# Kernel optimization log

Hardware: AMD Instinct MI355X
Metric: run time of the kernel (lower is better)

## Reference

```python
import jax, jax.numpy as jnp
import numpy as np

NUM_HEADS = 16
INACTIVE = 4          # cfg_comp.attention_heads_inactive
SIG_DIM = 64          # cfg_comp.attention_heads_signature_dim
MLP_HIDDEN = 512      # cfg_comp.attention_heads_inference_mlp_hidden


def setup_inputs() -> dict:
    key = jax.random.key(0)
    ks = jax.random.split(key, 16)
    S, B, E = 2048, 2, 1024
    def xavier(k, shape, gain=1.0):
        fan_in, fan_out = shape[1], shape[0]
        a = gain * np.sqrt(6.0 / (fan_in + fan_out))
        return jax.random.uniform(k, shape, jnp.float32, -a, a)
    g = 1.0 / np.sqrt(2.0)
    return {
        "query": jax.random.normal(ks[0], (S, B, E), jnp.float32),
        "q_w": xavier(ks[1], (E, E), g), "q_b": jnp.zeros((E,), jnp.float32),
        "k_w": xavier(ks[2], (E, E), g), "k_b": jnp.zeros((E,), jnp.float32),
        "v_w": xavier(ks[3], (E, E), g), "v_b": jnp.zeros((E,), jnp.float32),
        "out_w": xavier(ks[4], (E, E)), "out_b": jnp.zeros((E,), jnp.float32),
        "inf1_w": xavier(ks[5], (MLP_HIDDEN, E), np.sqrt(2.0)),
        "inf1_b": jnp.zeros((MLP_HIDDEN,), jnp.float32),
        "inf2_w": xavier(ks[6], (SIG_DIM, MLP_HIDDEN), np.sqrt(2.0)),
        "inf2_b": jnp.zeros((SIG_DIM,), jnp.float32),
        "head_sig": jax.random.normal(ks[7], (NUM_HEADS, SIG_DIM), jnp.float32)
                    * np.sqrt(2.0 / (NUM_HEADS + SIG_DIM)),
    }


def _head_mask(query, inf1_w, inf1_b, inf2_w, inf2_b, head_sig):
    # inference_masking_step: (S, B, E) -> binary mask (B, H, S)
    t = jax.nn.relu(query @ inf1_w.T + inf1_b)          # (S, B, hidden)
    t = t @ inf2_w.T + inf2_b                            # (S, B, sig)
    s = t @ head_sig.T                                   # (S, B, H) head scores
    keep = NUM_HEADS - INACTIVE
    kth = jax.lax.top_k(s, keep)[0][..., -1]             # (S, B) kth-largest score
    mask = (s >= kth[..., None]).astype(query.dtype)     # 1 at top-`keep` heads
    mask = jax.lax.stop_gradient(mask)                   # scatter of constants in torch
    return jnp.transpose(mask, (1, 2, 0))                # (B, H, S)


def reference(query, q_w, q_b, k_w, k_b, v_w, v_b, out_w, out_b,
              inf1_w, inf1_b, inf2_w, inf2_b, head_sig):
    S, B, E = query.shape
    H, D = NUM_HEADS, E // NUM_HEADS
    scaling = D ** (-0.5)

    q = (query @ q_w.T + q_b) * scaling                  # (S, B, E)
    k = query @ k_w.T + k_b
    v = query @ v_w.T + v_b
    # (S, B, E) -> (B, H, S, D)
    to_bhsd = lambda x: jnp.transpose(x.reshape(S, B, H, D), (1, 2, 0, 3))
    q, k, v = to_bhsd(q), to_bhsd(k), to_bhsd(v)

    attn = jax.nn.softmax(jnp.einsum("bhqd,bhkd->bhqk", q, k), axis=-1)
    o = jnp.einsum("bhqk,bhkd->bhqd", attn, v)           # (B, H, S, D)

    mask = _head_mask(query, inf1_w, inf1_b, inf2_w, inf2_b, head_sig)  # (B, H, S)
    o = o * mask[..., None]                              # gate per head per position

    out = jnp.transpose(o, (2, 0, 1, 3)).reshape(S, B, E)
    return out @ out_w.T + out_b
```

## Files before the change

kernel.cpp:

```cpp
#include <hip/hip_runtime.h>
#include <hip/hip_bf16.h>

#define S_LEN 2048
#define BATCH 2
#define EDIM 1024
#define NHEAD 16
#define DHEAD 64
#define HIDDEN 512
#define SIGD 64
#define KEEP 12

typedef __attribute__((ext_vector_type(8))) short bf16x8;
typedef __attribute__((ext_vector_type(4))) float f32x4;

static __device__ __forceinline__ float bf2f(short s) {
  unsigned int u = ((unsigned int)(unsigned short)s) << 16;
  float f; __builtin_memcpy(&f, &u, 4); return f;
}
static __device__ __forceinline__ short f2bf(float f) {
  unsigned int u; __builtin_memcpy(&u, &f, 4);
  u += 0x7fffu + ((u >> 16) & 1u);
  return (short)(u >> 16);
}

#if __has_builtin(__builtin_amdgcn_exp2f)
static __device__ __forceinline__ float fexp2(float x) { return __builtin_amdgcn_exp2f(x); }
#else
static __device__ __forceinline__ float fexp2(float x) { return exp2f(x); }
#endif

static __device__ __forceinline__ void gl_lds16(const short* g, short* l) {
  __builtin_amdgcn_global_load_lds(
      (const __attribute__((address_space(1))) unsigned int*)g,
      (__attribute__((address_space(3))) unsigned int*)l, 16, 0, 0);
}

template<int CTRL>
static __device__ __forceinline__ float dpp_movf(float x) {
  return __builtin_bit_cast(float, __builtin_amdgcn_update_dpp(
      0, __builtin_bit_cast(int, x), CTRL, 0xF, 0xF, true));
}
static __device__ __forceinline__ float row_max16(float v) {
  v = fmaxf(v, dpp_movf<0x128>(v));
  v = fmaxf(v, dpp_movf<0x124>(v));
  v = fmaxf(v, dpp_movf<0x122>(v));
  v = fmaxf(v, dpp_movf<0x121>(v));
  return v;
}
static __device__ __forceinline__ float row_sum16(float v) {
  v += dpp_movf<0x128>(v);
  v += dpp_movf<0x124>(v);
  v += dpp_movf<0x122>(v);
  v += dpp_movf<0x121>(v);
  return v;
}

__global__ __launch_bounds__(256) void cvt_all(
    const float* __restrict__ query, const float* __restrict__ inf1_w,
    const float* __restrict__ qw, const float* __restrict__ kw,
    const float* __restrict__ vw, const float* __restrict__ ow,
    short* __restrict__ qh, short* __restrict__ ql,
    short* __restrict__ w1h, short* __restrict__ w1l,
    short* __restrict__ Wq, short* __restrict__ Wk,
    short* __restrict__ Wv, short* __restrict__ Wo)
{
  int blk = blockIdx.x;
  if (blk < 4608) {
    const float* in; short *oh, *ol; int i;
    if (blk < 4096) { in = query;  oh = qh;  ol = ql;  i = (blk * 256 + threadIdx.x) * 4; }
    else            { in = inf1_w; oh = w1h; ol = w1l; i = ((blk - 4096) * 256 + threadIdx.x) * 4; }
    float4 f = *(const float4*)(in + i);
    union { short s[4]; uint2 v; } uh, ul;
    float x[4] = {f.x, f.y, f.z, f.w};
    #pragma unroll
    for (int u = 0; u < 4; ++u) {
      short h = f2bf(x[u]);
      uh.s[u] = h;
      ul.s[u] = f2bf(x[u] - bf2f(h));
    }
    *(uint2*)(oh + i) = uh.v;
    *(uint2*)(ol + i) = ul.v;
  } else {
    int t = blk - 4608;
    int mat = t >> 10, sub = t & 1023;
    const float* in = (mat == 0) ? qw : (mat == 1) ? kw : (mat == 2) ? vw : ow;
    short* out      = (mat == 0) ? Wq : (mat == 1) ? Wk : (mat == 2) ? Wv : Wo;
    int i = (sub * 256 + threadIdx.x) * 4;
    float4 f = *(const float4*)(in + i);
    union { short s[4]; uint2 v; } u;
    u.s[0] = f2bf(f.x); u.s[1] = f2bf(f.y); u.s[2] = f2bf(f.z); u.s[3] = f2bf(f.w);
    *(uint2*)(out + i) = u.v;
  }
}

template<bool F32OUT>
static __device__ __forceinline__ void gemm128_body(
    short* smem,
    const short* __restrict__ A, const short* __restrict__ B,
    const float* __restrict__ bias, void* __restrict__ outv,
    int row0, int col0, float scale)
{
  short* As = smem;
  short* Bs = smem + 128*32;
  const int tid  = threadIdx.x;
  const int wave = tid >> 6, lane = tid & 63;
  const int quad = lane >> 4, l16 = lane & 15;
  const int wr = wave >> 1, wc = wave & 1;
  const int lr = lane >> 2, lc8 = (lane & 3) * 8;

  const short* gA = A + (size_t)(row0 + wave*16 + lr) * EDIM + lc8;
  const short* gB = B + (size_t)(col0 + wave*16 + lr) * EDIM + lc8;
  short* lA = As + wave*512;
  short* lB = Bs + wave*512;

  f32x4 acc[4][4] = {};
  gl_lds16(gA, lA);  gl_lds16(gA + 64*EDIM, lA + 64*32);
  gl_lds16(gB, lB);  gl_lds16(gB + 64*EDIM, lB + 64*32);

  for (int k0 = 0; k0 < EDIM; k0 += 32) {
    __syncthreads();
    bf16x8 af[4], bfr[4];
    #pragma unroll
    for (int i = 0; i < 4; ++i)
      af[i] = *(const bf16x8*)&As[(wr*64 + i*16 + l16)*32 + quad*8];
    #pragma unroll
    for (int j = 0; j < 4; ++j)
      bfr[j] = *(const bf16x8*)&Bs[(wc*64 + j*16 + l16)*32 + quad*8];
    __syncthreads();
    if (k0 + 32 < EDIM) {
      const short* gA2 = gA + k0 + 32;
      const short* gB2 = gB + k0 + 32;
      gl_lds16(gA2, lA);  gl_lds16(gA2 + 64*EDIM, lA + 64*32);
      gl_lds16(gB2, lB);  gl_lds16(gB2 + 64*EDIM, lB + 64*32);
    }
    #pragma unroll
    for (int i = 0; i < 4; ++i)
      #pragma unroll
      for (int j = 0; j < 4; ++j)
        acc[i][j] = __builtin_amdgcn_mfma_f32_16x16x32_bf16(af[i], bfr[j], acc[i][j], 0, 0, 0);
  }
  #pragma unroll
  for (int j = 0; j < 4; ++j) {
    int col = col0 + wc*64 + j*16 + l16;
    float bv = bias[col];
    #pragma unroll
    for (int i = 0; i < 4; ++i) {
      int rowb = row0 + wr*64 + i*16 + quad*4;
      #pragma unroll
      for (int r = 0; r < 4; ++r) {
        float v = (acc[i][j][r] + bv) * scale;
        if constexpr (F32OUT) {
          ((float*)outv)[(size_t)(rowb + r) * EDIM + col] = v;
        } else {
          ((short*)outv)[(size_t)(rowb + r) * EDIM + col] = f2bf(v);
        }
      }
    }
  }
}

static __device__ __forceinline__ void gemm_t1_body(
    short* smem,
    const short* __restrict__ Agh, const short* __restrict__ Agl,
    const short* __restrict__ Bgh, const short* __restrict__ Bgl,
    const float* __restrict__ bias, float* __restrict__ T1,
    int row0, int col0)
{
  short* Ah = smem;
  short* Al = smem + 4096;
  short* Bh = smem + 8192;
  short* Bl = smem + 10240;
  const int tid  = threadIdx.x;
  const int wave = tid >> 6, lane = tid & 63;
  const int quad = lane >> 4, l16 = lane & 15;
  const int wr = wave >> 1, wc = wave & 1;
  const int lr = lane >> 2, lc8 = (lane & 3) * 8;

  const short* gAh = Agh + (size_t)(row0 + wave*16 + lr) * EDIM + lc8;
  const short* gAl = Agl + (size_t)(row0 + wave*16 + lr) * EDIM + lc8;
  const short* gBh = Bgh + (size_t)(col0 + wave*16 + lr) * EDIM + lc8;
  const short* gBl = Bgl + (size_t)(col0 + wave*16 + lr) * EDIM + lc8;
  short* lAh = Ah + wave*512;  short* lAl = Al + wave*512;
  short* lBh = Bh + wave*512;  short* lBl = Bl + wave*512;

  f32x4 acc[4][2] = {};
  gl_lds16(gAh, lAh);  gl_lds16(gAh + 64*EDIM, lAh + 64*32);
  gl_lds16(gAl, lAl);  gl_lds16(gAl + 64*EDIM, lAl + 64*32);
  gl_lds16(gBh, lBh);  gl_lds16(gBl, lBl);

  for (int k0 = 0; k0 < EDIM; k0 += 32) {
    __syncthreads();
    bf16x8 ah[4], al[4], bh[2], bl[2];
    #pragma unroll
    for (int i = 0; i < 4; ++i) {
      ah[i] = *(const bf16x8*)&Ah[(wr*64 + i*16 + l16)*32 + quad*8];
      al[i] = *(const bf16x8*)&Al[(wr*64 + i*16 + l16)*32 + quad*8];
    }
    #pragma unroll
    for (int j = 0; j < 2; ++j) {
      bh[j] = *(const bf16x8*)&Bh[(wc*32 + j*16 + l16)*32 + quad*8];
      bl[j] = *(const bf16x8*)&Bl[(wc*32 + j*16 + l16)*32 + quad*8];
    }
    __syncthreads();
    if (k0 + 32 < EDIM) {
      const short* p;
      p = gAh + k0 + 32;  gl_lds16(p, lAh);  gl_lds16(p + 64*EDIM, lAh + 64*32);
      p = gAl + k0 + 32;  gl_lds16(p, lAl);  gl_lds16(p + 64*EDIM, lAl + 64*32);
      gl_lds16(gBh + k0 + 32, lBh);  gl_lds16(gBl + k0 + 32, lBl);
    }
    #pragma unroll
    for (int i = 0; i < 4; ++i)
      #pragma unroll
      for (int j = 0; j < 2; ++j) {
        acc[i][j] = __builtin_amdgcn_mfma_f32_16x16x32_bf16(ah[i], bh[j], acc[i][j], 0, 0, 0);
        acc[i][j] = __builtin_amdgcn_mfma_f32_16x16x32_bf16(ah[i], bl[j], acc[i][j], 0, 0, 0);
        acc[i][j] = __builtin_amdgcn_mfma_f32_16x16x32_bf16(al[i], bh[j], acc[i][j], 0, 0, 0);
      }
  }
  #pragma unroll
  for (int j = 0; j < 2; ++j) {
    int col = col0 + wc*32 + j*16 + l16;
    float bv = bias[col];
    #pragma unroll
    for (int i = 0; i < 4; ++i) {
      int rowb = row0 + wr*64 + i*16 + quad*4;
      #pragma unroll
      for (int r = 0; r < 4; ++r)
        T1[(size_t)(rowb + r) * HIDDEN + col] = fmaxf(acc[i][j][r] + bv, 0.0f);
    }
  }
}

__global__ __launch_bounds__(256) void mega_gemm1(
    const short* __restrict__ qh, const short* __restrict__ ql,
    const short* __restrict__ w1h, const short* __restrict__ w1l,
    const float* __restrict__ inf1_b, float* __restrict__ T1,
    const short* __restrict__ Wq, const short* __restrict__ Wk,
    const short* __restrict__ Wv,
    const float* __restrict__ qb, const float* __restrict__ kb,
    const float* __restrict__ vb,
    short* __restrict__ Qp, short* __restrict__ Kp, short* __restrict__ Vp)
{
  __shared__ __attribute__((aligned(16))) short smem[12288];
  int blk = blockIdx.x;
  if ((blk & 3) == 3) {
    int id = blk >> 2;
    gemm_t1_body(smem, qh, ql, w1h, w1l, inf1_b, T1,
                 (id & 31) * 128, (id >> 5) * 64);
  } else {
    int id = (blk >> 2) * 3 + (blk & 3);
    int row0 = (id & 31) * 128;
    int rest = id >> 5;
    int mat = rest >> 3, cb = rest & 7;
    const short* B   = (mat == 0) ? Wq : (mat == 1) ? Wk : Wv;
    const float* bia = (mat == 0) ? qb : (mat == 1) ? kb : vb;
    short* out       = (mat == 0) ? Qp : (mat == 1) ? Kp : Vp;
    float scale      = (mat == 0) ? 0.18033688011112042f : 1.0f;
    gemm128_body<false>(smem, qh, B, bia, (void*)out, row0, cb * 128, scale);
  }
}

__global__ __launch_bounds__(256) void mid_kernel(
    const float* __restrict__ T1, const float* __restrict__ inf2_w,
    const float* __restrict__ inf2_b, const float* __restrict__ head_sig,
    float* __restrict__ maskbuf,
    const short* __restrict__ Vp, short* __restrict__ VT)
{
  __shared__ __attribute__((aligned(16))) float fsm[16*HIDDEN + 16*SIGD + 16*NHEAD];
  int blk = blockIdx.x;
  const int tid = threadIdx.x;
  if (blk < 256) {
    float (*t1s)[HIDDEN] = (float(*)[HIDDEN])fsm;
    float (*t2s)[SIGD]   = (float(*)[SIGD])(fsm + 16*HIDDEN);
    float (*ss)[NHEAD]   = (float(*)[NHEAD])(fsm + 16*HIDDEN + 16*SIGD);
    const int tok0 = blk * 16;
    {
      int row = tid >> 4, c0 = (tid & 15) * 32;
      const float* src = T1 + (size_t)(tok0 + row) * HIDDEN + c0;
      #pragma unroll
      for (int u = 0; u < 8; ++u)
        *(float4*)&t1s[row][c0 + u*4] = *(const float4*)(src + u*4);
    }
    __syncthreads();
    #pragma unroll
    for (int it = 0; it < 4; ++it) {
      int idx = tid + it * 256;
      int tok = idx >> 6, j = idx & 63;
      const float4* w4 = (const float4*)(inf2_w + (size_t)j * HIDDEN);
      const float4* t4 = (const float4*)(&t1s[tok][0]);
      float a = inf2_b[j];
      for (int k = 0; k < HIDDEN/4; ++k) {
        float4 wv = w4[k], tv = t4[k];
        a += tv.x*wv.x + tv.y*wv.y + tv.z*wv.z + tv.w*wv.w;
      }
      t2s[tok][j] = a;
    }
    __syncthreads();
    {
      int tok = tid >> 4, h = tid & 15;
      float a = 0.f;
      for (int d = 0; d < SIGD; ++d) a += t2s[tok][d] * head_sig[h*SIGD + d];
      ss[tok][h] = a;
    }
    __syncthreads();
    {
      int tok = tid >> 4, h = tid & 15;
      float sv = ss[tok][h];
      int cnt = 0;
      #pragma unroll
      for (int j = 0; j < NHEAD; ++j) cnt += (ss[tok][j] > sv) ? 1 : 0;
      int gt = tok0 + tok;
      int s = gt >> 1, b = gt & 1;
      maskbuf[((size_t)(b*NHEAD + h)) * S_LEN + s] = (cnt < KEEP) ? 1.0f : 0.0f;
    }
  } else {
    short (*tile)[72] = (short(*)[72])fsm;
    int t = blk - 256;
    const int s0 = (t & 31) * 64, e0 = ((t >> 5) & 15) * 64, b = t >> 9;
    {
      int sr = tid >> 2, ec = (tid & 3) * 16;
      const short* src = Vp + (size_t)(s0 + sr) * 2048 + b * 1024 + e0 + ec;
      *(uint4*)&tile[sr][ec]     = *(const uint4*)src;
      *(uint4*)&tile[sr][ec + 8] = *(const uint4*)(src + 8);
    }
    __syncthreads();
    {
      int er = tid >> 2, sc = (tid & 3) * 16;
      unsigned pack[8];
      #pragma unroll
      for (int u = 0; u < 8; ++u) {
        unsigned lo = (unsigned short)tile[sc + 2*u][er];
        unsigned hi = (unsigned short)tile[sc + 2*u + 1][er];
        pack[u] = lo | (hi << 16);
      }
      short* dst = VT + (size_t)(b * 1024 + e0 + er) * 2048 + s0 + sc;
      *(uint4*)(dst)     = *(uint4*)&pack[0];
      *(uint4*)(dst + 8) = *(uint4*)&pack[4];
    }
  }
}

__global__ __launch_bounds__(256) void flash_attn(
    short* QpOg, const short* __restrict__ Kp, const short* __restrict__ VT,
    const float* __restrict__ maskbuf)
{
  __shared__ __attribute__((aligned(16))) short Ks[128][68];
  __shared__ __attribute__((aligned(16))) short Vt[2][64][68];
  __shared__ __attribute__((aligned(16))) short uni[8704];
  const int bh = blockIdx.x;
  const int b = bh >> 4, h = bh & 15;
  const int q0 = blockIdx.y * 64;
  const int tid = threadIdx.x;
  const int wave = tid >> 6, lane = tid & 63;
  const int quad = lane >> 4, l16 = lane & 15;
  const size_t colbase = (size_t)b * EDIM + h * DHEAD;
  const size_t rstride = (size_t)BATCH * EDIM;

  const int r4 = tid >> 2, c16 = (tid & 3) * 16;
  const short* gK = Kp + (size_t)r4 * rstride + colbase + c16;
  const short* gV = VT + (size_t)(bh * 64 + r4) * S_LEN + c16;

  {
    const short* src = QpOg + (size_t)(q0 + r4) * rstride + colbase + c16;
    *(uint4*)&uni[r4*68 + c16]     = *(const uint4*)src;
    *(uint4*)&uni[r4*68 + c16 + 8] = *(const uint4*)(src + 8);
  }
  __syncthreads();
  bf16x8 aq0 = *(const bf16x8*)&uni[(wave*16 + l16)*68 + quad*8];
  bf16x8 aq1 = *(const bf16x8*)&uni[(wave*16 + l16)*68 + 32 + quad*8];
  short* Psw = &uni[wave * 2176];

  uint4 ka0 = *(const uint4*)(gK);
  uint4 ka1 = *(const uint4*)(gK + 8);
  uint4 kb0 = *(const uint4*)(gK + 64*rstride);
  uint4 kb1 = *(const uint4*)(gK + 64*rstride + 8);
  uint4 va0 = *(const uint4*)(gV);
  uint4 va1 = *(const uint4*)(gV + 8);
  uint4 vb0 = *(const uint4*)(gV + 64);
  uint4 vb1 = *(const uint4*)(gV + 72);

  float m_i[4], l_i[4];
  f32x4 oacc[4];
  #pragma unroll
  for (int r = 0; r < 4; ++r) { m_i[r] = -1e30f; l_i[r] = 0.f; }
  #pragma unroll
  for (int dt = 0; dt < 4; ++dt) oacc[dt] = f32x4{0.f, 0.f, 0.f, 0.f};

  for (int kv0 = 0; kv0 < S_LEN; kv0 += 128) {
    __syncthreads();
    *(uint4*)&Ks[r4][c16]        = ka0;
    *(uint4*)&Ks[r4][c16 + 8]    = ka1;
    *(uint4*)&Ks[r4+64][c16]     = kb0;
    *(uint4*)&Ks[r4+64][c16 + 8] = kb1;
    *(uint4*)&Vt[0][r4][c16]     = va0;
    *(uint4*)&Vt[0][r4][c16 + 8] = va1;
    *(uint4*)&Vt[1][r4][c16]     = vb0;
    *(uint4*)&Vt[1][r4][c16 + 8] = vb1;
    __syncthreads();
    if (kv0 + 128 < S_LEN) {
      const short* nK = gK + (size_t)(kv0 + 128) * rstride;
      const short* nV = gV + (kv0 + 128);
      ka0 = *(const uint4*)nK;
      ka1 = *(const uint4*)(nK + 8);
      kb0 = *(const uint4*)(nK + 64*rstride);
      kb1 = *(const uint4*)(nK + 64*rstride + 8);
      va0 = *(const uint4*)nV;
      va1 = *(const uint4*)(nV + 8);
      vb0 = *(const uint4*)(nV + 64);
      vb1 = *(const uint4*)(nV + 72);
    }
    f32x4 sacc[8];
    #pragma unroll
    for (int c = 0; c < 8; ++c) sacc[c] = f32x4{0.f, 0.f, 0.f, 0.f};
    __builtin_amdgcn_s_setprio(1);
    #pragma unroll
    for (int c = 0; c < 8; ++c) {
      bf16x8 b0 = *(const bf16x8*)&Ks[c*16 + l16][quad*8];
      bf16x8 b1 = *(const bf16x8*)&Ks[c*16 + l16][32 + quad*8];
      sacc[c] = __builtin_amdgcn_mfma_f32_16x16x32_bf16(aq0, b0, sacc[c], 0, 0, 0);
      sacc[c] = __builtin_amdgcn_mfma_f32_16x16x32_bf16(aq1, b1, sacc[c], 0, 0, 0);
    }
    __builtin_amdgcn_s_setprio(0);
    #pragma unroll
    for (int r = 0; r < 4; ++r) {
      float vmax = fmaxf(fmaxf(fmaxf(sacc[0][r], sacc[1][r]),
                               fmaxf(sacc[2][r], sacc[3][r])),
                         fmaxf(fmaxf(sacc[4][r], sacc[5][r]),
                               fmaxf(sacc[6][r], sacc[7][r])));
      vmax = row_max16(vmax);
      if (!__all(vmax <= m_i[r] + 8.0f)) {
        float mnew = fmaxf(m_i[r], vmax);
        float alpha = fexp2(m_i[r] - mnew);
        l_i[r] *= alpha;
        #pragma unroll
        for (int dt = 0; dt < 4; ++dt) oacc[dt][r] *= alpha;
        m_i[r] = mnew;
      }
      float rsum = 0.f;
      short* prow = &Psw[(quad*4 + r)*68 + l16];
      #pragma unroll
      for (int p = 0; p < 4; ++p) {
        float ea = fexp2(sacc[2*p][r]   - m_i[r]);
        float eb = fexp2(sacc[2*p+1][r] - m_i[r]);
        unsigned pk = __builtin_amdgcn_perm(
            __builtin_bit_cast(unsigned, eb),
            __builtin_bit_cast(unsigned, ea), 0x07060302u);
        short* pr = prow + (p >> 1) * 1088;
        pr[(2*(p & 1))*16]     = (short)(pk & 0xffffu);
        pr[(2*(p & 1) + 1)*16] = (short)(pk >> 16);
        rsum += ea + eb;
      }
      rsum = row_sum16(rsum);
      l_i[r] += rsum;
    }
    asm volatile("s_waitcnt lgkmcnt(0)" ::: "memory");
    __builtin_amdgcn_s_setprio(1);
    #pragma unroll
    for (int ks = 0; ks < 4; ++ks) {
      bf16x8 ap = *(const bf16x8*)&Psw[(ks>>1)*1088 + l16*68 + (ks&1)*32 + quad*8];
      #pragma unroll
      for (int dt = 0; dt < 4; ++dt) {
        bf16x8 bb = *(const bf16x8*)&Vt[ks>>1][dt*16 + l16][(ks&1)*32 + quad*8];
        oacc[dt] = __builtin_amdgcn_mfma_f32_16x16x32_bf16(ap, bb, oacc[dt], 0, 0, 0);
      }
    }
    __builtin_amdgcn_s_setprio(0);
  }
  #pragma unroll
  for (int r = 0; r < 4; ++r) {
    int s = q0 + wave*16 + quad*4 + r;
    float mk = maskbuf[((size_t)(b*NHEAD + h)) * S_LEN + s];
    float scale = mk / l_i[r];
    short* dst = QpOg + (size_t)s * rstride + colbase;
    #pragma unroll
    for (int dt = 0; dt < 4; ++dt)
      dst[dt*16 + l16] = f2bf(oacc[dt][r] * scale);
  }
}

__global__ __launch_bounds__(256) void gemm_out(
    const short* __restrict__ A, const short* __restrict__ W,
    const float* __restrict__ bias, float* __restrict__ out)
{
  __shared__ __attribute__((aligned(16))) short smem[8192];
  gemm128_body<true>(smem, A, W, bias, (void*)out,
                     blockIdx.x * 128, blockIdx.y * 128, 1.0f);
}

extern "C" void kernel_launch(void* const* d_in, const int* in_sizes, int n_in,
                              void* d_out, int out_size, void* d_ws, size_t ws_size,
                              hipStream_t stream)
{
  const float* query   = (const float*)d_in[0];
  const float* q_w     = (const float*)d_in[1];
  const float* q_b     = (const float*)d_in[2];
  const float* k_w     = (const float*)d_in[3];
  const float* k_b     = (const float*)d_in[4];
  const float* v_w     = (const float*)d_in[5];
  const float* v_b     = (const float*)d_in[6];
  const float* out_w   = (const float*)d_in[7];
  const float* out_b   = (const float*)d_in[8];
  const float* inf1_w  = (const float*)d_in[9];
  const float* inf1_b  = (const float*)d_in[10];
  const float* inf2_w  = (const float*)d_in[11];
  const float* inf2_b  = (const float*)d_in[12];
  const float* head_sig= (const float*)d_in[13];

  char* ws = (char*)d_ws;
  short* qh      = (short*)(ws);
  short* VTb     = (short*)(ws);
  short* ql      = (short*)(ws + (size_t)( 8u<<20));
  float* maskbuf = (float*)(ws + (size_t)( 8u<<20));
  short* Qp      = (short*)(ws + (size_t)(16u<<20));
  short* Kp      = (short*)(ws + (size_t)(24u<<20));
  short* Vp      = (short*)(ws + (size_t)(32u<<20));
  short* Wo      = (short*)(ws + (size_t)(40u<<20));
  char* ob = (char*)d_out;
  float* T1  = (float*)(ob);
  short* w1h = (short*)(ob + (size_t)( 8u<<20));
  short* w1l = (short*)(ob + (size_t)( 9u<<20));
  short* Wq  = (short*)(ob + (size_t)(10u<<20));
  short* Wk  = (short*)(ob + (size_t)(12u<<20));
  short* Wv  = (short*)(ob + (size_t)(14u<<20));
  float* out = (float*)d_out;

  dim3 blk(256);
  cvt_all<<<dim3(8704), blk, 0, stream>>>(query, inf1_w, q_w, k_w, v_w, out_w,
                                          qh, ql, w1h, w1l, Wq, Wk, Wv, Wo);
  mega_gemm1<<<dim3(1024), blk, 0, stream>>>(qh, ql, w1h, w1l, inf1_b, T1,
                                             Wq, Wk, Wv, q_b, k_b, v_b, Qp, Kp, Vp);
  mid_kernel<<<dim3(1280), blk, 0, stream>>>(T1, inf2_w, inf2_b, head_sig, maskbuf,
                                             Vp, VTb);
  flash_attn<<<dim3(32, 32), blk, 0, stream>>>(Qp, Kp, VTb, maskbuf);
  gemm_out<<<dim3(32, 8), blk, 0, stream>>>(Qp, Wo, out_b, out);
}
```

Measured before the change: 361.0 us.

## Drop register prefetch of K/V tiles and lazy softmax rescale in attention loop

Removes the register-based prefetch of the next K/V tile, so each iteration now loads its tile from global memory directly before storing it to LDS. It also drops the conditional lazy-rescale (skip when the max grew by less than 8) and always rescales the running max, sum and output accumulators. This lowers register pressure and removes the warp-vote branch, but exposes global load latency that the prefetch used to hide and adds an exp and multiplies every iteration.

```diff
diff --git a/kernel.cpp b/kernel.cpp
--- a/kernel.cpp
+++ b/kernel.cpp
@@ -370,15 +370,6 @@
   bf16x8 aq1 = *(const bf16x8*)&uni[(wave*16 + l16)*68 + 32 + quad*8];
   short* Psw = &uni[wave * 2176];
 
-  uint4 ka0 = *(const uint4*)(gK);
-  uint4 ka1 = *(const uint4*)(gK + 8);
-  uint4 kb0 = *(const uint4*)(gK + 64*rstride);
-  uint4 kb1 = *(const uint4*)(gK + 64*rstride + 8);
-  uint4 va0 = *(const uint4*)(gV);
-  uint4 va1 = *(const uint4*)(gV + 8);
-  uint4 vb0 = *(const uint4*)(gV + 64);
-  uint4 vb1 = *(const uint4*)(gV + 72);
-
   float m_i[4], l_i[4];
   f32x4 oacc[4];
   #pragma unroll
@@ -388,27 +379,27 @@
 
   for (int kv0 = 0; kv0 < S_LEN; kv0 += 128) {
     __syncthreads();
-    *(uint4*)&Ks[r4][c16]        = ka0;
-    *(uint4*)&Ks[r4][c16 + 8]    = ka1;
-    *(uint4*)&Ks[r4+64][c16]     = kb0;
-    *(uint4*)&Ks[r4+64][c16 + 8] = kb1;
-    *(uint4*)&Vt[0][r4][c16]     = va0;
-    *(uint4*)&Vt[0][r4][c16 + 8] = va1;
-    *(uint4*)&Vt[1][r4][c16]     = vb0;
-    *(uint4*)&Vt[1][r4][c16 + 8] = vb1;
-    __syncthreads();
-    if (kv0 + 128 < S_LEN) {
-      const short* nK = gK + (size_t)(kv0 + 128) * rstride;
-      const short* nV = gV + (kv0 + 128);
-      ka0 = *(const uint4*)nK;
-      ka1 = *(const uint4*)(nK + 8);
-      kb0 = *(const uint4*)(nK + 64*rstride);
-      kb1 = *(const uint4*)(nK + 64*rstride + 8);
-      va0 = *(const uint4*)nV;
-      va1 = *(const uint4*)(nV + 8);
-      vb0 = *(const uint4*)(nV + 64);
-      vb1 = *(const uint4*)(nV + 72);
-    }
+    {
+      const short* nK = gK + (size_t)kv0 * rstride;
+      const short* nV = gV + kv0;
+      uint4 ka0 = *(const uint4*)nK;
+      uint4 ka1 = *(const uint4*)(nK + 8);
+      uint4 kb0 = *(const uint4*)(nK + 64*rstride);
+      uint4 kb1 = *(const uint4*)(nK + 64*rstride + 8);
+      uint4 va0 = *(const uint4*)nV;
+      uint4 va1 = *(const uint4*)(nV + 8);
+      uint4 vb0 = *(const uint4*)(nV + 64);
+      uint4 vb1 = *(const uint4*)(nV + 72);
+      *(uint4*)&Ks[r4][c16]        = ka0;
+      *(uint4*)&Ks[r4][c16 + 8]    = ka1;
+      *(uint4*)&Ks[r4+64][c16]     = kb0;
+      *(uint4*)&Ks[r4+64][c16 + 8] = kb1;
+      *(uint4*)&Vt[0][r4][c16]     = va0;
+      *(uint4*)&Vt[0][r4][c16 + 8] = va1;
+      *(uint4*)&Vt[1][r4][c16]     = vb0;
+      *(uint4*)&Vt[1][r4][c16 + 8] = vb1;
+    }
+    __syncthreads();
     f32x4 sacc[8];
     #pragma unroll
     for (int c = 0; c < 8; ++c) sacc[c] = f32x4{0.f, 0.f, 0.f, 0.f};
@@ -428,20 +419,14 @@
                          fmaxf(fmaxf(sacc[4][r], sacc[5][r]),
                                fmaxf(sacc[6][r], sacc[7][r])));
       vmax = row_max16(vmax);
-      if (!__all(vmax <= m_i[r] + 8.0f)) {
-        float mnew = fmaxf(m_i[r], vmax);
-        float alpha = fexp2(m_i[r] - mnew);
-        l_i[r] *= alpha;
-        #pragma unroll
-        for (int dt = 0; dt < 4; ++dt) oacc[dt][r] *= alpha;
-        m_i[r] = mnew;
-      }
+      float mnew = fmaxf(m_i[r], vmax);
+      float alpha = fexp2(m_i[r] - mnew);
       float rsum = 0.f;
       short* prow = &Psw[(quad*4 + r)*68 + l16];
       #pragma unroll
       for (int p = 0; p < 4; ++p) {
-        float ea = fexp2(sacc[2*p][r]   - m_i[r]);
-        float eb = fexp2(sacc[2*p+1][r] - m_i[r]);
+        float ea = fexp2(sacc[2*p][r]   - mnew);
+        float eb = fexp2(sacc[2*p+1][r] - mnew);
         unsigned pk = __builtin_amdgcn_perm(
             __builtin_bit_cast(unsigned, eb),
             __builtin_bit_cast(unsigned, ea), 0x07060302u);
@@ -451,7 +436,10 @@
         rsum += ea + eb;
       }
       rsum = row_sum16(rsum);
-      l_i[r] += rsum;
+      l_i[r] = l_i[r] * alpha + rsum;
+      m_i[r] = mnew;
+      #pragma unroll
+      for (int dt = 0; dt < 4; ++dt) oacc[dt][r] *= alpha;
     }
     asm volatile("s_waitcnt lgkmcnt(0)" ::: "memory");
     __builtin_amdgcn_s_setprio(1);
```

Result: no change. 354.1 us (-1.9%).
